# Kernel optimization log

Hardware: AMD Instinct MI355X
Metric: run time of the kernel (lower is better)

## Reference

```python
import jax, jax.numpy as jnp
import numpy as np

LN_EPS = 1e-5
NORM_EPS = 1e-12
SLOPE = 0.1

def _layernorm(x, g, b):
    m = jnp.mean(x, axis=-1, keepdims=True)
    v = jnp.mean(jnp.square(x - m), axis=-1, keepdims=True)
    return (x - m) * jax.lax.rsqrt(v + LN_EPS) * g + b

def _leaky(x):
    return jnp.where(x >= 0, x, SLOPE * x)

def setup_inputs() -> dict:
    key = jax.random.key(0)
    ks = jax.random.split(key, 8)
    N = 1048576
    features = jax.random.normal(ks[0], (N, 128), dtype=jnp.float32)
    # PyTorch Linear default init: U(-1/sqrt(fan_in), 1/sqrt(fan_in))
    W1 = jax.random.uniform(ks[1], (32, 128), jnp.float32, -1/np.sqrt(128), 1/np.sqrt(128))
    g1 = jnp.ones((32,), jnp.float32); b1 = jnp.zeros((32,), jnp.float32)
    W2 = jax.random.uniform(ks[2], (16, 32), jnp.float32, -1/np.sqrt(32), 1/np.sqrt(32))
    g2 = jnp.ones((16,), jnp.float32); b2 = jnp.zeros((16,), jnp.float32)
    W3 = jax.random.uniform(ks[3], (3, 16), jnp.float32, -1/np.sqrt(16), 1/np.sqrt(16))
    b3 = jax.random.uniform(ks[4], (3,), jnp.float32, -1/np.sqrt(16), 1/np.sqrt(16))
    return {"features": features, "W1": W1, "g1": g1, "b1": b1,
            "W2": W2, "g2": g2, "b2": b2, "W3": W3, "b3": b3}

def reference(features, W1, g1, b1, W2, g2, b2, W3, b3):
    x = features @ W1.T                       # [N,32]
    x = _leaky(_layernorm(x, g1, b1))
    x = x @ W2.T                               # [N,16]
    x = _leaky(_layernorm(x, g2, b2))
    x = x @ W3.T + b3                          # [N,3]
    # F.normalize(dim=-1): x / max(||x||_2, eps)
    n = jnp.linalg.norm(x, axis=-1, keepdims=True)
    return x / jnp.maximum(n, NORM_EPS)
```

## Files before the change

kernel.cpp:

```cpp
#include <hip/hip_runtime.h>
#include <math.h>

typedef short bf16x8 __attribute__((ext_vector_type(8)));
typedef float f32x4  __attribute__((ext_vector_type(4)));
typedef float f32x2  __attribute__((ext_vector_type(2)));

#define TPB 256
#define GRID 768
#define CSTRIDE 36
#define BFR_BYTES 16384
#define CT_BYTES (256 * CSTRIDE * 4)
#define BOFF(nt, ks, p) ((((nt)*4 + (ks))*2 + (p))*256)

#define PKFMA(a, b, c) __builtin_elementwise_fma((a), (b), (c))

__device__ __forceinline__ unsigned cvt_pk_bf16(float lo, float hi) {
    unsigned r;
    asm("v_cvt_pk_bf16_f32 %0, %1, %2" : "=v"(r) : "v"(lo), "v"(hi));
    return r;
}
__device__ __forceinline__ void split2pk(float x0, float x1, unsigned &p, unsigned &q) {
    p = cvt_pk_bf16(x0, x1);
    f32x2 xv = {x0, x1};
    f32x2 fv = {__uint_as_float(p << 16), __uint_as_float(p & 0xffff0000u)};
    f32x2 r = xv - fv;
    q = cvt_pk_bf16(r.x, r.y);
}
__device__ __forceinline__ f32x2 leaky2(f32x2 y) {
    const f32x2 zero = {0.f, 0.f};
    const f32x2 slope = {0.1f, 0.1f};
    return PKFMA(__builtin_elementwise_min(y, zero), slope,
                 __builtin_elementwise_max(y, zero));
}

__device__ __forceinline__ void load_tile(float4* dst, const float* __restrict__ feat,
                                          unsigned rbase, int arow, int acol, unsigned nm1) {
    unsigned rr = rbase + arow;
    rr = rr < nm1 ? rr : nm1;
    const float* ap = feat + (size_t)rr * 128 + acol;
#pragma unroll
    for (int ks = 0; ks < 4; ++ks) {
        dst[2 * ks]     = *(const float4*)(ap + ks * 32);
        dst[2 * ks + 1] = *(const float4*)(ap + ks * 32 + 4);
    }
}

__global__ __launch_bounds__(TPB, 3) void decoder_kernel(
    const float* __restrict__ feat,
    const float* __restrict__ W1, const float* __restrict__ g1, const float* __restrict__ b1,
    const float* __restrict__ W2, const float* __restrict__ g2, const float* __restrict__ b2,
    const float* __restrict__ W3, const float* __restrict__ b3,
    float* __restrict__ out, int N, unsigned nchunks)
{
    __shared__ __align__(16) unsigned char lds[BFR_BYTES + CT_BYTES];
    unsigned* bfr = (unsigned*)lds;

    const int t = threadIdx.x;
    const int l = t & 63;
    const int w = t >> 6;
    const int arow = l & 15;
    const int acol = (l >> 4) * 8;
    const unsigned nm1 = (unsigned)(N - 1);
    float* myCt = (float*)(lds + BFR_BYTES) + w * 64 * CSTRIDE;

    const unsigned wid = blockIdx.x * 4 + w;
    const unsigned NW  = GRID * 4;

    float4 buf[2][8];
    unsigned c = wid;
    if (c < nchunks) load_tile(buf[0], feat, c * 64, arow, acol, nm1);

    for (int cc = t; cc < 512; cc += 256) {
        const int lc = cc & 63, ks = (cc >> 6) & 3, nt = (cc >> 8) & 1;
        const float* wp = W1 + (nt * 16 + (lc & 15)) * 128 + ks * 32 + (lc >> 4) * 8;
        float v[8];
        *(float4*)(v)     = *(const float4*)(wp);
        *(float4*)(v + 4) = *(const float4*)(wp + 4);
        unsigned p[4], q[4];
#pragma unroll
        for (int i = 0; i < 4; ++i) split2pk(v[2*i], v[2*i+1], p[i], q[i]);
        uint4 q1 = {p[0], p[1], p[2], p[3]};
        uint4 q2 = {q[0], q[1], q[2], q[3]};
        *(uint4*)(bfr + BOFF(nt, ks, 0) + lc * 4) = q1;
        *(uint4*)(bfr + BOFF(nt, ks, 1) + lc * 4) = q2;
    }
    __syncthreads();

    for (; c < nchunks; c += NW) {
        const unsigned base = c * 64;

#pragma unroll
        for (int j = 0; j < 4; ++j) {
            if (j < 3) {
                load_tile(buf[(j + 1) & 1], feat, base + (j + 1) * 16, arow, acol, nm1);
            } else {
                const unsigned cn = c + NW;
                if (cn < nchunks)
                    load_tile(buf[0], feat, cn * 64, arow, acol, nm1);
            }
            f32x4 acc0 = {0.f, 0.f, 0.f, 0.f};
            f32x4 acc1 = {0.f, 0.f, 0.f, 0.f};
#pragma unroll
            for (int ks = 0; ks < 4; ++ks) {
                float v[8];
                *(float4*)(v)     = buf[j & 1][2 * ks];
                *(float4*)(v + 4) = buf[j & 1][2 * ks + 1];
                unsigned p[4], q[4];
#pragma unroll
                for (int i = 0; i < 4; ++i) split2pk(v[2*i], v[2*i+1], p[i], q[i]);
                uint4 q1 = {p[0], p[1], p[2], p[3]};
                uint4 q2 = {q[0], q[1], q[2], q[3]};
                bf16x8 a1 = __builtin_bit_cast(bf16x8, q1);
                bf16x8 a2 = __builtin_bit_cast(bf16x8, q2);
                bf16x8 B10 = __builtin_bit_cast(bf16x8, *(const uint4*)(bfr + BOFF(0, ks, 0) + l * 4));
                bf16x8 B20 = __builtin_bit_cast(bf16x8, *(const uint4*)(bfr + BOFF(0, ks, 1) + l * 4));
                bf16x8 B11 = __builtin_bit_cast(bf16x8, *(const uint4*)(bfr + BOFF(1, ks, 0) + l * 4));
                bf16x8 B21 = __builtin_bit_cast(bf16x8, *(const uint4*)(bfr + BOFF(1, ks, 1) + l * 4));
                acc0 = __builtin_amdgcn_mfma_f32_16x16x32_bf16(a1, B10, acc0, 0, 0, 0);
                acc1 = __builtin_amdgcn_mfma_f32_16x16x32_bf16(a1, B11, acc1, 0, 0, 0);
                acc0 = __builtin_amdgcn_mfma_f32_16x16x32_bf16(a2, B10, acc0, 0, 0, 0);
                acc1 = __builtin_amdgcn_mfma_f32_16x16x32_bf16(a2, B11, acc1, 0, 0, 0);
                acc0 = __builtin_amdgcn_mfma_f32_16x16x32_bf16(a1, B20, acc0, 0, 0, 0);
                acc1 = __builtin_amdgcn_mfma_f32_16x16x32_bf16(a1, B21, acc1, 0, 0, 0);
            }
            const int crow = j * 16 + (l >> 4) * 4;
            const int ccol = l & 15;
#pragma unroll
            for (int r = 0; r < 4; ++r) {
                myCt[(crow + r) * CSTRIDE + ccol]      = acc0[r];
                myCt[(crow + r) * CSTRIDE + 16 + ccol] = acc1[r];
            }
        }

        f32x2 xp[16];
#pragma unroll
        for (int cc = 0; cc < 8; ++cc) {
            const float4 v = *(const float4*)(myCt + l * CSTRIDE + cc * 4);
            xp[2 * cc]     = f32x2{v.x, v.y};
            xp[2 * cc + 1] = f32x2{v.z, v.w};
        }

        f32x2 sv = xp[0];
#pragma unroll
        for (int i = 1; i < 16; ++i) sv += xp[i];
        const float m = (sv.x + sv.y) * (1.f / 32.f);
        const f32x2 mv = {m, m};
        f32x2 vv = {0.f, 0.f};
#pragma unroll
        for (int i = 0; i < 16; ++i) { const f32x2 d = xp[i] - mv; vv = PKFMA(d, d, vv); }
        const float rs1 = rsqrtf((vv.x + vv.y) * (1.f / 32.f) + 1e-5f);
        const f32x2 rs1v = {rs1, rs1};

        f32x2 zp[16];
#pragma unroll
        for (int i = 0; i < 16; ++i) {
            const f32x2 gb = *(const f32x2*)(g1 + 2 * i);
            const f32x2 bb = *(const f32x2*)(b1 + 2 * i);
            zp[i] = leaky2(PKFMA((xp[i] - mv) * rs1v, gb, bb));
        }

        float a2v[16];
#pragma unroll
        for (int k = 0; k < 16; ++k) {
            const float* __restrict__ wrow = W2 + k * 32;
            f32x2 acc = {0.f, 0.f};
#pragma unroll
            for (int jj = 0; jj < 16; ++jj)
                acc = PKFMA(zp[jj], *(const f32x2*)(wrow + 2 * jj), acc);
            a2v[k] = acc.x + acc.y;
        }

        f32x2 a2p[8];
#pragma unroll
        for (int i = 0; i < 8; ++i) a2p[i] = f32x2{a2v[2 * i], a2v[2 * i + 1]};

        f32x2 s2 = a2p[0];
#pragma unroll
        for (int i = 1; i < 8; ++i) s2 += a2p[i];
        const float m2 = (s2.x + s2.y) * (1.f / 16.f);
        const f32x2 m2v = {m2, m2};
        f32x2 v2v = {0.f, 0.f};
#pragma unroll
        for (int i = 0; i < 8; ++i) { const f32x2 d = a2p[i] - m2v; v2v = PKFMA(d, d, v2v); }
        const float rs2 = rsqrtf((v2v.x + v2v.y) * (1.f / 16.f) + 1e-5f);
        const f32x2 rs2v = {rs2, rs2};

        f32x2 z2p[8];
#pragma unroll
        for (int i = 0; i < 8; ++i) {
            const f32x2 gb = *(const f32x2*)(g2 + 2 * i);
            const f32x2 bb = *(const f32x2*)(b2 + 2 * i);
            z2p[i] = leaky2(PKFMA((a2p[i] - m2v) * rs2v, gb, bb));
        }

        float o[3];
#pragma unroll
        for (int q = 0; q < 3; ++q) {
            const float* __restrict__ wrow = W3 + q * 16;
            f32x2 acc = {0.f, 0.f};
#pragma unroll
            for (int jj = 0; jj < 8; ++jj)
                acc = PKFMA(z2p[jj], *(const f32x2*)(wrow + 2 * jj), acc);
            o[q] = b3[q] + acc.x + acc.y;
        }
        const float nrm = sqrtf(o[0]*o[0] + o[1]*o[1] + o[2]*o[2]);
        const float inv = 1.f / fmaxf(nrm, 1e-12f);

        const size_t myrow = (size_t)base + l;
        if (myrow < (size_t)N) {
            out[myrow * 3 + 0] = o[0] * inv;
            out[myrow * 3 + 1] = o[1] * inv;
            out[myrow * 3 + 2] = o[2] * inv;
        }
    }
}

extern "C" void kernel_launch(void* const* d_in, const int* in_sizes, int n_in,
                              void* d_out, int out_size, void* d_ws, size_t ws_size,
                              hipStream_t stream) {
    const float* feat = (const float*)d_in[0];
    const float* W1   = (const float*)d_in[1];
    const float* g1   = (const float*)d_in[2];
    const float* b1   = (const float*)d_in[3];
    const float* W2   = (const float*)d_in[4];
    const float* g2   = (const float*)d_in[5];
    const float* b2   = (const float*)d_in[6];
    const float* W3   = (const float*)d_in[7];
    const float* b3   = (const float*)d_in[8];
    float* out = (float*)d_out;

    const int N = in_sizes[0] / 128;
    const unsigned nchunks = (unsigned)((N + 63) / 64);

    decoder_kernel<<<GRID, TPB, 0, stream>>>(feat, W1, g1, b1, W2, g2, b2, W3, b3,
                                             out, N, nchunks);
}
```

Before: 112.7 us.

## Deepen feature-tile prefetch to three rotating register buffers

Moves from a double-buffered register prefetch to a triple-buffered rotation, so two 16-row tiles are in flight ahead of the one being computed. The chunk loop is unrolled three times with the buffer roles rotated, which keeps the register arrays statically indexed. The goal is to hide more global-memory latency on this bandwidth-bound streaming kernel. In exchange it holds 8 more float4 registers per thread, which may raise register pressure under launch_bounds(256,3) and cause spills, and the code size grows.

```diff
diff --git a/kernel.cpp b/kernel.cpp
--- a/kernel.cpp
+++ b/kernel.cpp
@@ -7,6 +7,7 @@
 
 #define TPB 256
 #define GRID 768
+#define NW   (GRID * 4)
 #define CSTRIDE 36
 #define BFR_BYTES 16384
 #define CT_BYTES (256 * CSTRIDE * 4)
@@ -33,7 +34,7 @@
                  __builtin_elementwise_max(y, zero));
 }
 
-__device__ __forceinline__ void load_tile(float4* dst, const float* __restrict__ feat,
+__device__ __forceinline__ void load_tile(float4 (&dst)[8], const float* __restrict__ feat,
                                           unsigned rbase, int arow, int acol, unsigned nm1) {
     unsigned rr = rbase + arow;
     rr = rr < nm1 ? rr : nm1;
@@ -44,6 +45,165 @@
         dst[2 * ks + 1] = *(const float4*)(ap + ks * 32 + 4);
     }
 }
+
+__device__ __forceinline__ void do_tile(const float4 (&S)[8], const unsigned* bfr, int l,
+                                        f32x4 &acc0, f32x4 &acc1) {
+#pragma unroll
+    for (int ks = 0; ks < 4; ++ks) {
+        float v[8];
+        *(float4*)(v)     = S[2 * ks];
+        *(float4*)(v + 4) = S[2 * ks + 1];
+        unsigned p[4], q[4];
+#pragma unroll
+        for (int i = 0; i < 4; ++i) split2pk(v[2*i], v[2*i+1], p[i], q[i]);
+        uint4 q1 = {p[0], p[1], p[2], p[3]};
+        uint4 q2 = {q[0], q[1], q[2], q[3]};
+        bf16x8 a1 = __builtin_bit_cast(bf16x8, q1);
+        bf16x8 a2 = __builtin_bit_cast(bf16x8, q2);
+        bf16x8 B10 = __builtin_bit_cast(bf16x8, *(const uint4*)(bfr + BOFF(0, ks, 0) + l * 4));
+        bf16x8 B20 = __builtin_bit_cast(bf16x8, *(const uint4*)(bfr + BOFF(0, ks, 1) + l * 4));
+        bf16x8 B11 = __builtin_bit_cast(bf16x8, *(const uint4*)(bfr + BOFF(1, ks, 0) + l * 4));
+        bf16x8 B21 = __builtin_bit_cast(bf16x8, *(const uint4*)(bfr + BOFF(1, ks, 1) + l * 4));
+        acc0 = __builtin_amdgcn_mfma_f32_16x16x32_bf16(a1, B10, acc0, 0, 0, 0);
+        acc1 = __builtin_amdgcn_mfma_f32_16x16x32_bf16(a1, B11, acc1, 0, 0, 0);
+        acc0 = __builtin_amdgcn_mfma_f32_16x16x32_bf16(a2, B10, acc0, 0, 0, 0);
+        acc1 = __builtin_amdgcn_mfma_f32_16x16x32_bf16(a2, B11, acc1, 0, 0, 0);
+        acc0 = __builtin_amdgcn_mfma_f32_16x16x32_bf16(a1, B20, acc0, 0, 0, 0);
+        acc1 = __builtin_amdgcn_mfma_f32_16x16x32_bf16(a1, B21, acc1, 0, 0, 0);
+    }
+}
+
+__device__ __forceinline__ void ct_write(float* myCt, int j, int l,
+                                         const f32x4 &a0, const f32x4 &a1) {
+    const int crow = j * 16 + ((l >> 4) << 2);
+    const int ccol = l & 15;
+#pragma unroll
+    for (int r = 0; r < 4; ++r) {
+        myCt[(crow + r) * CSTRIDE + ccol]      = a0[r];
+        myCt[(crow + r) * CSTRIDE + 16 + ccol] = a1[r];
+    }
+}
+
+__device__ __forceinline__ void tail_store(
+    const float* myCt, int l, unsigned base,
+    const float* __restrict__ g1, const float* __restrict__ b1,
+    const float* __restrict__ W2, const float* __restrict__ g2, const float* __restrict__ b2,
+    const float* __restrict__ W3, const float* __restrict__ b3,
+    float* __restrict__ out, int N)
+{
+    f32x2 xp[16];
+#pragma unroll
+    for (int cc = 0; cc < 8; ++cc) {
+        const float4 v = *(const float4*)(myCt + l * CSTRIDE + cc * 4);
+        xp[2 * cc]     = f32x2{v.x, v.y};
+        xp[2 * cc + 1] = f32x2{v.z, v.w};
+    }
+
+    f32x2 sv = xp[0];
+#pragma unroll
+    for (int i = 1; i < 16; ++i) sv += xp[i];
+    const float m = (sv.x + sv.y) * (1.f / 32.f);
+    const f32x2 mv = {m, m};
+    f32x2 vv = {0.f, 0.f};
+#pragma unroll
+    for (int i = 0; i < 16; ++i) { const f32x2 d = xp[i] - mv; vv = PKFMA(d, d, vv); }
+    const float rs1 = rsqrtf((vv.x + vv.y) * (1.f / 32.f) + 1e-5f);
+    const f32x2 rs1v = {rs1, rs1};
+
+    f32x2 zp[16];
+#pragma unroll
+    for (int i = 0; i < 16; ++i) {
+        const f32x2 gb = *(const f32x2*)(g1 + 2 * i);
+        const f32x2 bb = *(const f32x2*)(b1 + 2 * i);
+        zp[i] = leaky2(PKFMA((xp[i] - mv) * rs1v, gb, bb));
+    }
+
+    float a2v[16];
+#pragma unroll
+    for (int k = 0; k < 16; ++k) {
+        const float* __restrict__ wrow = W2 + k * 32;
+        f32x2 acc = {0.f, 0.f};
+#pragma unroll
+        for (int jj = 0; jj < 16; ++jj)
+            acc = PKFMA(zp[jj], *(const f32x2*)(wrow + 2 * jj), acc);
+        a2v[k] = acc.x + acc.y;
+    }
+
+    f32x2 a2p[8];
+#pragma unroll
+    for (int i = 0; i < 8; ++i) a2p[i] = f32x2{a2v[2 * i], a2v[2 * i + 1]};
+
+    f32x2 s2 = a2p[0];
+#pragma unroll
+    for (int i = 1; i < 8; ++i) s2 += a2p[i];
+    const float m2 = (s2.x + s2.y) * (1.f / 16.f);
+    const f32x2 m2v = {m2, m2};
+    f32x2 v2v = {0.f, 0.f};
+#pragma unroll
+    for (int i = 0; i < 8; ++i) { const f32x2 d = a2p[i] - m2v; v2v = PKFMA(d, d, v2v); }
+    const float rs2 = rsqrtf((v2v.x + v2v.y) * (1.f / 16.f) + 1e-5f);
+    const f32x2 rs2v = {rs2, rs2};
+
+    f32x2 z2p[8];
+#pragma unroll
+    for (int i = 0; i < 8; ++i) {
+        const f32x2 gb = *(const f32x2*)(g2 + 2 * i);
+        const f32x2 bb = *(const f32x2*)(b2 + 2 * i);
+        z2p[i] = leaky2(PKFMA((a2p[i] - m2v) * rs2v, gb, bb));
+    }
+
+    float o[3];
+#pragma unroll
+    for (int q = 0; q < 3; ++q) {
+        const float* __restrict__ wrow = W3 + q * 16;
+        f32x2 acc = {0.f, 0.f};
+#pragma unroll
+        for (int jj = 0; jj < 8; ++jj)
+            acc = PKFMA(z2p[jj], *(const f32x2*)(wrow + 2 * jj), acc);
+        o[q] = b3[q] + acc.x + acc.y;
+    }
+    const float nrm = sqrtf(o[0]*o[0] + o[1]*o[1] + o[2]*o[2]);
+    const float inv = 1.f / fmaxf(nrm, 1e-12f);
+
+    const size_t myrow = (size_t)base + l;
+    if (myrow < (size_t)N) {
+        out[myrow * 3 + 0] = o[0] * inv;
+        out[myrow * 3 + 1] = o[1] * inv;
+        out[myrow * 3 + 2] = o[2] * inv;
+    }
+}
+
+#define CHUNK_BODY(SA, SB, SC)                                                \
+    {                                                                         \
+        const unsigned base = c * 64;                                         \
+        const unsigned cn   = c + NW;                                         \
+        const bool hn = (cn < nchunks);                                       \
+        {                            \
+            load_tile(SC, feat, base + 32, arow, acol, nm1);                  \
+            f32x4 a0 = {0,0,0,0}, a1 = {0,0,0,0};                             \
+            do_tile(SA, bfr, l, a0, a1);                                      \
+            ct_write(myCt, 0, l, a0, a1);                                     \
+        }                                                                     \
+        {                            \
+            load_tile(SA, feat, base + 48, arow, acol, nm1);                  \
+            f32x4 a0 = {0,0,0,0}, a1 = {0,0,0,0};                             \
+            do_tile(SB, bfr, l, a0, a1);                                      \
+            ct_write(myCt, 1, l, a0, a1);                                     \
+        }                                                                     \
+        {                       \
+            if (hn) load_tile(SB, feat, cn * 64, arow, acol, nm1);            \
+            f32x4 a0 = {0,0,0,0}, a1 = {0,0,0,0};                             \
+            do_tile(SC, bfr, l, a0, a1);                                      \
+            ct_write(myCt, 2, l, a0, a1);                                     \
+        }                                                                     \
+        {                       \
+            if (hn) load_tile(SC, feat, cn * 64 + 16, arow, acol, nm1);       \
+            f32x4 a0 = {0,0,0,0}, a1 = {0,0,0,0};                             \
+            do_tile(SA, bfr, l, a0, a1);                                      \
+            ct_write(myCt, 3, l, a0, a1);                                     \
+        }                                                                     \
+        tail_store(myCt, l, base, g1, b1, W2, g2, b2, W3, b3, out, N);        \
+    }
 
 __global__ __launch_bounds__(TPB, 3) void decoder_kernel(
     const float* __restrict__ feat,
@@ -64,11 +224,13 @@
     float* myCt = (float*)(lds + BFR_BYTES) + w * 64 * CSTRIDE;
 
     const unsigned wid = blockIdx.x * 4 + w;
-    const unsigned NW  = GRID * 4;
-
-    float4 buf[2][8];
+
+    float4 s0[8], s1[8], s2[8];
     unsigned c = wid;
-    if (c < nchunks) load_tile(buf[0], feat, c * 64, arow, acol, nm1);
+    if (c < nchunks) {
+        load_tile(s0, feat, c * 64, arow, acol, nm1);
+        load_tile(s1, feat, c * 64 + 16, arow, acol, nm1);
+    }
 
     for (int cc = t; cc < 512; cc += 256) {
         const int lc = cc & 63, ks = (cc >> 6) & 3, nt = (cc >> 8) & 1;
@@ -86,132 +248,13 @@
     }
     __syncthreads();
 
-    for (; c < nchunks; c += NW) {
-        const unsigned base = c * 64;
-
-#pragma unroll
-        for (int j = 0; j < 4; ++j) {
-            if (j < 3) {
-                load_tile(buf[(j + 1) & 1], feat, base + (j + 1) * 16, arow, acol, nm1);
-            } else {
-                const unsigned cn = c + NW;
-                if (cn < nchunks)
-                    load_tile(buf[0], feat, cn * 64, arow, acol, nm1);
-            }
-            f32x4 acc0 = {0.f, 0.f, 0.f, 0.f};
-            f32x4 acc1 = {0.f, 0.f, 0.f, 0.f};
-#pragma unroll
-            for (int ks = 0; ks < 4; ++ks) {
-                float v[8];
-                *(float4*)(v)     = buf[j & 1][2 * ks];
-                *(float4*)(v + 4) = buf[j & 1][2 * ks + 1];
-                unsigned p[4], q[4];
-#pragma unroll
-                for (int i = 0; i < 4; ++i) split2pk(v[2*i], v[2*i+1], p[i], q[i]);
-                uint4 q1 = {p[0], p[1], p[2], p[3]};
-                uint4 q2 = {q[0], q[1], q[2], q[3]};
-                bf16x8 a1 = __builtin_bit_cast(bf16x8, q1);
-                bf16x8 a2 = __builtin_bit_cast(bf16x8, q2);
-                bf16x8 B10 = __builtin_bit_cast(bf16x8, *(const uint4*)(bfr + BOFF(0, ks, 0) + l * 4));
-                bf16x8 B20 = __builtin_bit_cast(bf16x8, *(const uint4*)(bfr + BOFF(0, ks, 1) + l * 4));
-                bf16x8 B11 = __builtin_bit_cast(bf16x8, *(const uint4*)(bfr + BOFF(1, ks, 0) + l * 4));
-                bf16x8 B21 = __builtin_bit_cast(bf16x8, *(const uint4*)(bfr + BOFF(1, ks, 1) + l * 4));
-                acc0 = __builtin_amdgcn_mfma_f32_16x16x32_bf16(a1, B10, acc0, 0, 0, 0);
-                acc1 = __builtin_amdgcn_mfma_f32_16x16x32_bf16(a1, B11, acc1, 0, 0, 0);
-                acc0 = __builtin_amdgcn_mfma_f32_16x16x32_bf16(a2, B10, acc0, 0, 0, 0);
-                acc1 = __builtin_amdgcn_mfma_f32_16x16x32_bf16(a2, B11, acc1, 0, 0, 0);
-                acc0 = __builtin_amdgcn_mfma_f32_16x16x32_bf16(a1, B20, acc0, 0, 0, 0);
-                acc1 = __builtin_amdgcn_mfma_f32_16x16x32_bf16(a1, B21, acc1, 0, 0, 0);
-            }
-            const int crow = j * 16 + (l >> 4) * 4;
-            const int ccol = l & 15;
-#pragma unroll
-            for (int r = 0; r < 4; ++r) {
-                myCt[(crow + r) * CSTRIDE + ccol]      = acc0[r];
-                myCt[(crow + r) * CSTRIDE + 16 + ccol] = acc1[r];
-            }
-        }
-
-        f32x2 xp[16];
-#pragma unroll
-        for (int cc = 0; cc < 8; ++cc) {
-            const float4 v = *(const float4*)(myCt + l * CSTRIDE + cc * 4);
-            xp[2 * cc]     = f32x2{v.x, v.y};
-            xp[2 * cc + 1] = f32x2{v.z, v.w};
-        }
-
-        f32x2 sv = xp[0];
-#pragma unroll
-        for (int i = 1; i < 16; ++i) sv += xp[i];
-        const float m = (sv.x + sv.y) * (1.f / 32.f);
-        const f32x2 mv = {m, m};
-        f32x2 vv = {0.f, 0.f};
-#pragma unroll
-        for (int i = 0; i < 16; ++i) { const f32x2 d = xp[i] - mv; vv = PKFMA(d, d, vv); }
-        const float rs1 = rsqrtf((vv.x + vv.y) * (1.f / 32.f) + 1e-5f);
-        const f32x2 rs1v = {rs1, rs1};
-
-        f32x2 zp[16];
-#pragma unroll
-        for (int i = 0; i < 16; ++i) {
-            const f32x2 gb = *(const f32x2*)(g1 + 2 * i);
-            const f32x2 bb = *(const f32x2*)(b1 + 2 * i);
-            zp[i] = leaky2(PKFMA((xp[i] - mv) * rs1v, gb, bb));
-        }
-
-        float a2v[16];
-#pragma unroll
-        for (int k = 0; k < 16; ++k) {
-            const float* __restrict__ wrow = W2 + k * 32;
-            f32x2 acc = {0.f, 0.f};
-#pragma unroll
-            for (int jj = 0; jj < 16; ++jj)
-                acc = PKFMA(zp[jj], *(const f32x2*)(wrow + 2 * jj), acc);
-            a2v[k] = acc.x + acc.y;
-        }
-
-        f32x2 a2p[8];
-#pragma unroll
-        for (int i = 0; i < 8; ++i) a2p[i] = f32x2{a2v[2 * i], a2v[2 * i + 1]};
-
-        f32x2 s2 = a2p[0];
-#pragma unroll
-        for (int i = 1; i < 8; ++i) s2 += a2p[i];
-        const float m2 = (s2.x + s2.y) * (1.f / 16.f);
-        const f32x2 m2v = {m2, m2};
-        f32x2 v2v = {0.f, 0.f};
-#pragma unroll
-        for (int i = 0; i < 8; ++i) { const f32x2 d = a2p[i] - m2v; v2v = PKFMA(d, d, v2v); }
-        const float rs2 = rsqrtf((v2v.x + v2v.y) * (1.f / 16.f) + 1e-5f);
-        const f32x2 rs2v = {rs2, rs2};
-
-        f32x2 z2p[8];
-#pragma unroll
-        for (int i = 0; i < 8; ++i) {
-            const f32x2 gb = *(const f32x2*)(g2 + 2 * i);
-            const f32x2 bb = *(const f32x2*)(b2 + 2 * i);
-            z2p[i] = leaky2(PKFMA((a2p[i] - m2v) * rs2v, gb, bb));
-        }
-
-        float o[3];
-#pragma unroll
-        for (int q = 0; q < 3; ++q) {
-            const float* __restrict__ wrow = W3 + q * 16;
-            f32x2 acc = {0.f, 0.f};
-#pragma unroll
-            for (int jj = 0; jj < 8; ++jj)
-                acc = PKFMA(z2p[jj], *(const f32x2*)(wrow + 2 * jj), acc);
-            o[q] = b3[q] + acc.x + acc.y;
-        }
-        const float nrm = sqrtf(o[0]*o[0] + o[1]*o[1] + o[2]*o[2]);
-        const float inv = 1.f / fmaxf(nrm, 1e-12f);
-
-        const size_t myrow = (size_t)base + l;
-        if (myrow < (size_t)N) {
-            out[myrow * 3 + 0] = o[0] * inv;
-            out[myrow * 3 + 1] = o[1] * inv;
-            out[myrow * 3 + 2] = o[2] * inv;
-        }
+    while (c < nchunks) {
+        CHUNK_BODY(s0, s1, s2)
+        c += NW; if (c >= nchunks) break;
+        CHUNK_BODY(s1, s2, s0)
+        c += NW; if (c >= nchunks) break;
+        CHUNK_BODY(s2, s0, s1)
+        c += NW;
     }
 }
 
```

Measured after the change: 179.2 us. 1.59x slower.

## Shrink per-wave chunk to 32 rows and raise occupancy with a larger grid

Applied to the files above, without the earlier changes.

Each wave now processes 32-row chunks, held in two 16-row register tiles, instead of 64-row chunks. The next chunk's loads are issued right after each tile's MFMA pass, so both prefetches are in flight during the epilogue. The smaller chunk shrinks the LDS staging buffer and register arrays, which allows launch bounds of 4 blocks per CU and a grid of 1024 blocks, aiming to hide more memory latency. In exchange, the per-row scalar epilogue (layernorms, small matmuls, normalize) now runs with only half the lanes doing useful work, which roughly doubles the epilogue ALU cost per row.

```diff
diff --git a/kernel.cpp b/kernel.cpp
--- a/kernel.cpp
+++ b/kernel.cpp
@@ -6,10 +6,12 @@
 typedef float f32x2  __attribute__((ext_vector_type(2)));
 
 #define TPB 256
-#define GRID 768
+#define GRID 1024
+#define NW   (GRID * 4)
+#define CROWS 32
 #define CSTRIDE 36
 #define BFR_BYTES 16384
-#define CT_BYTES (256 * CSTRIDE * 4)
+#define CT_BYTES (4 * CROWS * CSTRIDE * 4)
 #define BOFF(nt, ks, p) ((((nt)*4 + (ks))*2 + (p))*256)
 
 #define PKFMA(a, b, c) __builtin_elementwise_fma((a), (b), (c))
@@ -33,7 +35,7 @@
                  __builtin_elementwise_max(y, zero));
 }
 
-__device__ __forceinline__ void load_tile(float4* dst, const float* __restrict__ feat,
+__device__ __forceinline__ void load_tile(float4 (&dst)[8], const float* __restrict__ feat,
                                           unsigned rbase, int arow, int acol, unsigned nm1) {
     unsigned rr = rbase + arow;
     rr = rr < nm1 ? rr : nm1;
@@ -45,7 +47,45 @@
     }
 }
 
-__global__ __launch_bounds__(TPB, 3) void decoder_kernel(
+__device__ __forceinline__ void do_tile(const float4 (&S)[8], const unsigned* bfr, int l,
+                                        f32x4 &acc0, f32x4 &acc1) {
+#pragma unroll
+    for (int ks = 0; ks < 4; ++ks) {
+        float v[8];
+        *(float4*)(v)     = S[2 * ks];
+        *(float4*)(v + 4) = S[2 * ks + 1];
+        unsigned p[4], q[4];
+#pragma unroll
+        for (int i = 0; i < 4; ++i) split2pk(v[2*i], v[2*i+1], p[i], q[i]);
+        uint4 q1 = {p[0], p[1], p[2], p[3]};
+        uint4 q2 = {q[0], q[1], q[2], q[3]};
+        bf16x8 a1 = __builtin_bit_cast(bf16x8, q1);
+        bf16x8 a2 = __builtin_bit_cast(bf16x8, q2);
+        bf16x8 B10 = __builtin_bit_cast(bf16x8, *(const uint4*)(bfr + BOFF(0, ks, 0) + l * 4));
+        bf16x8 B20 = __builtin_bit_cast(bf16x8, *(const uint4*)(bfr + BOFF(0, ks, 1) + l * 4));
+        bf16x8 B11 = __builtin_bit_cast(bf16x8, *(const uint4*)(bfr + BOFF(1, ks, 0) + l * 4));
+        bf16x8 B21 = __builtin_bit_cast(bf16x8, *(const uint4*)(bfr + BOFF(1, ks, 1) + l * 4));
+        acc0 = __builtin_amdgcn_mfma_f32_16x16x32_bf16(a1, B10, acc0, 0, 0, 0);
+        acc1 = __builtin_amdgcn_mfma_f32_16x16x32_bf16(a1, B11, acc1, 0, 0, 0);
+        acc0 = __builtin_amdgcn_mfma_f32_16x16x32_bf16(a2, B10, acc0, 0, 0, 0);
+        acc1 = __builtin_amdgcn_mfma_f32_16x16x32_bf16(a2, B11, acc1, 0, 0, 0);
+        acc0 = __builtin_amdgcn_mfma_f32_16x16x32_bf16(a1, B20, acc0, 0, 0, 0);
+        acc1 = __builtin_amdgcn_mfma_f32_16x16x32_bf16(a1, B21, acc1, 0, 0, 0);
+    }
+}
+
+__device__ __forceinline__ void ct_write(float* myCt, int j, int l,
+                                         const f32x4 &a0, const f32x4 &a1) {
+    const int crow = j * 16 + ((l >> 4) << 2);
+    const int ccol = l & 15;
+#pragma unroll
+    for (int r = 0; r < 4; ++r) {
+        myCt[(crow + r) * CSTRIDE + ccol]      = a0[r];
+        myCt[(crow + r) * CSTRIDE + 16 + ccol] = a1[r];
+    }
+}
+
+__global__ __launch_bounds__(TPB, 4) void decoder_kernel(
     const float* __restrict__ feat,
     const float* __restrict__ W1, const float* __restrict__ g1, const float* __restrict__ b1,
     const float* __restrict__ W2, const float* __restrict__ g2, const float* __restrict__ b2,
@@ -61,14 +101,16 @@
     const int arow = l & 15;
     const int acol = (l >> 4) * 8;
     const unsigned nm1 = (unsigned)(N - 1);
-    float* myCt = (float*)(lds + BFR_BYTES) + w * 64 * CSTRIDE;
+    float* myCt = (float*)(lds + BFR_BYTES) + w * CROWS * CSTRIDE;
 
     const unsigned wid = blockIdx.x * 4 + w;
-    const unsigned NW  = GRID * 4;
-
-    float4 buf[2][8];
+
+    float4 s0[8], s1[8];
     unsigned c = wid;
-    if (c < nchunks) load_tile(buf[0], feat, c * 64, arow, acol, nm1);
+    if (c < nchunks) {
+        load_tile(s0, feat, c * CROWS, arow, acol, nm1);
+        load_tile(s1, feat, c * CROWS + 16, arow, acol, nm1);
+    }
 
     for (int cc = t; cc < 512; cc += 256) {
         const int lc = cc & 63, ks = (cc >> 6) & 3, nt = (cc >> 8) & 1;
@@ -87,55 +129,28 @@
     __syncthreads();
 
     for (; c < nchunks; c += NW) {
-        const unsigned base = c * 64;
-
-#pragma unroll
-        for (int j = 0; j < 4; ++j) {
-            if (j < 3) {
-                load_tile(buf[(j + 1) & 1], feat, base + (j + 1) * 16, arow, acol, nm1);
-            } else {
-                const unsigned cn = c + NW;
-                if (cn < nchunks)
-                    load_tile(buf[0], feat, cn * 64, arow, acol, nm1);
-            }
-            f32x4 acc0 = {0.f, 0.f, 0.f, 0.f};
-            f32x4 acc1 = {0.f, 0.f, 0.f, 0.f};
-#pragma unroll
-            for (int ks = 0; ks < 4; ++ks) {
-                float v[8];
-                *(float4*)(v)     = buf[j & 1][2 * ks];
-                *(float4*)(v + 4) = buf[j & 1][2 * ks + 1];
-                unsigned p[4], q[4];
-#pragma unroll
-                for (int i = 0; i < 4; ++i) split2pk(v[2*i], v[2*i+1], p[i], q[i]);
-                uint4 q1 = {p[0], p[1], p[2], p[3]};
-                uint4 q2 = {q[0], q[1], q[2], q[3]};
-                bf16x8 a1 = __builtin_bit_cast(bf16x8, q1);
-                bf16x8 a2 = __builtin_bit_cast(bf16x8, q2);
-                bf16x8 B10 = __builtin_bit_cast(bf16x8, *(const uint4*)(bfr + BOFF(0, ks, 0) + l * 4));
-                bf16x8 B20 = __builtin_bit_cast(bf16x8, *(const uint4*)(bfr + BOFF(0, ks, 1) + l * 4));
-                bf16x8 B11 = __builtin_bit_cast(bf16x8, *(const uint4*)(bfr + BOFF(1, ks, 0) + l * 4));
-                bf16x8 B21 = __builtin_bit_cast(bf16x8, *(const uint4*)(bfr + BOFF(1, ks, 1) + l * 4));
-                acc0 = __builtin_amdgcn_mfma_f32_16x16x32_bf16(a1, B10, acc0, 0, 0, 0);
-                acc1 = __builtin_amdgcn_mfma_f32_16x16x32_bf16(a1, B11, acc1, 0, 0, 0);
-                acc0 = __builtin_amdgcn_mfma_f32_16x16x32_bf16(a2, B10, acc0, 0, 0, 0);
-                acc1 = __builtin_amdgcn_mfma_f32_16x16x32_bf16(a2, B11, acc1, 0, 0, 0);
-                acc0 = __builtin_amdgcn_mfma_f32_16x16x32_bf16(a1, B20, acc0, 0, 0, 0);
-                acc1 = __builtin_amdgcn_mfma_f32_16x16x32_bf16(a1, B21, acc1, 0, 0, 0);
-            }
-            const int crow = j * 16 + (l >> 4) * 4;
-            const int ccol = l & 15;
-#pragma unroll
-            for (int r = 0; r < 4; ++r) {
-                myCt[(crow + r) * CSTRIDE + ccol]      = acc0[r];
-                myCt[(crow + r) * CSTRIDE + 16 + ccol] = acc1[r];
-            }
-        }
-
+        const unsigned base = c * CROWS;
+        const unsigned cn = c + NW;
+        const bool hn = (cn < nchunks);
+
+        {
+            f32x4 a0 = {0,0,0,0}, a1 = {0,0,0,0};
+            do_tile(s0, bfr, l, a0, a1);
+            ct_write(myCt, 0, l, a0, a1);
+            if (hn) load_tile(s0, feat, cn * CROWS, arow, acol, nm1);
+        }
+        {
+            f32x4 a0 = {0,0,0,0}, a1 = {0,0,0,0};
+            do_tile(s1, bfr, l, a0, a1);
+            ct_write(myCt, 1, l, a0, a1);
+            if (hn) load_tile(s1, feat, cn * CROWS + 16, arow, acol, nm1);
+        }
+
+        const int r = l & 31;
         f32x2 xp[16];
 #pragma unroll
         for (int cc = 0; cc < 8; ++cc) {
-            const float4 v = *(const float4*)(myCt + l * CSTRIDE + cc * 4);
+            const float4 v = *(const float4*)(myCt + r * CSTRIDE + cc * 4);
             xp[2 * cc]     = f32x2{v.x, v.y};
             xp[2 * cc + 1] = f32x2{v.z, v.w};
         }
@@ -151,12 +166,11 @@
         const float rs1 = rsqrtf((vv.x + vv.y) * (1.f / 32.f) + 1e-5f);
         const f32x2 rs1v = {rs1, rs1};
 
-        f32x2 zp[16];
 #pragma unroll
         for (int i = 0; i < 16; ++i) {
             const f32x2 gb = *(const f32x2*)(g1 + 2 * i);
             const f32x2 bb = *(const f32x2*)(b1 + 2 * i);
-            zp[i] = leaky2(PKFMA((xp[i] - mv) * rs1v, gb, bb));
+            xp[i] = leaky2(PKFMA((xp[i] - mv) * rs1v, gb, bb));
         }
 
         float a2v[16];
@@ -166,7 +180,7 @@
             f32x2 acc = {0.f, 0.f};
 #pragma unroll
             for (int jj = 0; jj < 16; ++jj)
-                acc = PKFMA(zp[jj], *(const f32x2*)(wrow + 2 * jj), acc);
+                acc = PKFMA(xp[jj], *(const f32x2*)(wrow + 2 * jj), acc);
             a2v[k] = acc.x + acc.y;
         }
 
@@ -185,12 +199,11 @@
         const float rs2 = rsqrtf((v2v.x + v2v.y) * (1.f / 16.f) + 1e-5f);
         const f32x2 rs2v = {rs2, rs2};
 
-        f32x2 z2p[8];
 #pragma unroll
         for (int i = 0; i < 8; ++i) {
             const f32x2 gb = *(const f32x2*)(g2 + 2 * i);
             const f32x2 bb = *(const f32x2*)(b2 + 2 * i);
-            z2p[i] = leaky2(PKFMA((a2p[i] - m2v) * rs2v, gb, bb));
+            a2p[i] = leaky2(PKFMA((a2p[i] - m2v) * rs2v, gb, bb));
         }
 
         float o[3];
@@ -200,14 +213,14 @@
             f32x2 acc = {0.f, 0.f};
 #pragma unroll
             for (int jj = 0; jj < 8; ++jj)
-                acc = PKFMA(z2p[jj], *(const f32x2*)(wrow + 2 * jj), acc);
+                acc = PKFMA(a2p[jj], *(const f32x2*)(wrow + 2 * jj), acc);
             o[q] = b3[q] + acc.x + acc.y;
         }
         const float nrm = sqrtf(o[0]*o[0] + o[1]*o[1] + o[2]*o[2]);
         const float inv = 1.f / fmaxf(nrm, 1e-12f);
 
-        const size_t myrow = (size_t)base + l;
-        if (myrow < (size_t)N) {
+        const size_t myrow = (size_t)base + r;
+        if (l < 32 && myrow < (size_t)N) {
             out[myrow * 3 + 0] = o[0] * inv;
             out[myrow * 3 + 1] = o[1] * inv;
             out[myrow * 3 + 2] = o[2] * inv;
@@ -230,7 +243,7 @@
     float* out = (float*)d_out;
 
     const int N = in_sizes[0] / 128;
-    const unsigned nchunks = (unsigned)((N + 63) / 64);
+    const unsigned nchunks = (unsigned)((N + CROWS - 1) / CROWS);
 
     decoder_kernel<<<GRID, TPB, 0, stream>>>(feat, W1, g1, b1, W2, g2, b2, W3, b3,
                                              out, N, nchunks);
```

After: 177.6 us. +57.6%, slower.
